# Optimization experiments

Measured on AMD Instinct MI355X. Metric: run time of the kernel, lower is better.

## Reference

```python
import jax, jax.numpy as jnp
import numpy as np

NUM_GRAPHS = 4096


def setup_inputs() -> dict:
    key = jax.random.key(0)
    k1, k2, k3, k4, k5 = jax.random.split(key, 5)
    N, H = 500000, 256
    x = jax.random.normal(k1, (N, H), dtype=jnp.float32)
    batch = jnp.sort(jax.random.randint(k2, (N,), 0, NUM_GRAPHS, dtype=jnp.int64))
    # gate MLP: Linear(H, H//2) -> tanh -> Linear(H//2, 1)
    W1 = jax.random.normal(k3, (H, H // 2), dtype=jnp.float32) / np.sqrt(H)
    b1 = jnp.zeros((H // 2,), dtype=jnp.float32)
    W2 = jax.random.normal(k4, (H // 2, 1), dtype=jnp.float32) / np.sqrt(H // 2)
    b2 = jnp.zeros((1,), dtype=jnp.float32)
    return {"x": x, "batch": batch, "W1": W1, "b1": b1, "W2": W2, "b2": b2}


def reference(x, batch, W1, b1, W2, b2):
    # gate scores per node: (N,)
    h = jnp.tanh(x @ W1 + b1)
    scores = (h @ W2 + b2).squeeze(-1)
    # segment (per-graph) softmax over nodes
    seg_max = jax.ops.segment_max(scores, batch, num_segments=NUM_GRAPHS)
    # empty segments give -inf max; guard so gather stays finite
    seg_max = jnp.where(jnp.isfinite(seg_max), seg_max, 0.0)
    ex = jnp.exp(scores - seg_max[batch])
    seg_sum = jax.ops.segment_sum(ex, batch, num_segments=NUM_GRAPHS)
    weights = ex / seg_sum[batch]  # (N,)
    # weighted scatter-add pooling -> (B, H)
    pooled = jax.ops.segment_sum(weights[:, None] * x, batch, num_segments=NUM_GRAPHS)
    return pooled, weights
```

## Files before the change

kernel.cpp:

```cpp
#include <hip/hip_runtime.h>
#include <hip/hip_bf16.h>

#define NGRAPH 4096

typedef __attribute__((ext_vector_type(8))) short s16x8;
typedef __attribute__((ext_vector_type(4))) float f32x4;
typedef unsigned int u32;

__device__ inline short f2bf(float f) {
  unsigned u = __float_as_uint(f);
  unsigned r = u + 0x7fffu + ((u >> 16) & 1u);
  return (short)(r >> 16);
}

__global__ void prepack_w1(const float* __restrict__ W1, s16x8* __restrict__ w1p) {
  int t = blockIdx.x * 256 + threadIdx.x;
  int f = t >> 6, l = t & 63;
  int kt = f >> 3, ct = f & 7;
  int k0 = kt * 32 + ((l >> 4) * 8);
  int c  = ct * 16 + (l & 15);
  s16x8 v;
  #pragma unroll
  for (int e = 0; e < 8; ++e) v[e] = f2bf(W1[(k0 + e) * 128 + c]);
  w1p[f * 64 + l] = v;
}

__device__ inline long long getb(const void* b, int i, int is64) {
  if (is64) return ((const long long*)b)[i];
  return (long long)((const int*)b)[i];
}

__device__ inline int lowb(const void* b, int n, long long v, int is64) {
  int lo = 0, hi = n;
  while (lo < hi) {
    int mid = (lo + hi) >> 1;
    if (getb(b, mid, is64) < v) lo = mid + 1; else hi = mid;
  }
  return lo;
}

__device__ inline int batch_is64(const void* batch, int N) {
  int probe = ((N & 1) == 0) ? (N - 1) : (N - 2);
  return (((const int*)batch)[probe] == 0) ? 1 : 0;
}

__global__ void seg_offsets(const void* __restrict__ batch, int* __restrict__ offs, int N) {
  int g = blockIdx.x * 256 + threadIdx.x;
  const int is64 = batch_is64(batch, N);
  if (g <= NGRAPH) offs[g] = lowb(batch, N, (long long)g, is64);
}

__device__ inline float fast_tanh(float v) {
  v = fminf(fmaxf(v, -15.f), 15.f);
  float e = __expf(2.f * v);
  return __fdividef(e - 1.f, e + 1.f);
}

__device__ inline void dma16(const float* src, char* ldsdst) {
  __builtin_amdgcn_global_load_lds(
      (const __attribute__((address_space(1))) u32*)src,
      (__attribute__((address_space(3))) u32*)ldsdst,
      16, 0, 0);
}

__global__ __launch_bounds__(256, 2)
void gate_pool(const float* __restrict__ x, const int* __restrict__ offs,
               const float* __restrict__ b1, const float* __restrict__ W2,
               const float* __restrict__ b2p, const s16x8* __restrict__ w1p,
               float* __restrict__ pooled, float* __restrict__ expout,
               float* __restrict__ segsum, int N)
{
  __shared__ __align__(16) char tile[64 * 1024];
  __shared__ float sp[2][64];
  __shared__ float sw[64];

  const int tid = threadIdx.x;
  const int w = tid >> 6, l = tid & 63;
  const int colhalf = w & 1, wp = w >> 1;
  const int l15 = l & 15, lg = l >> 4;
  const int node0 = blockIdx.x * 64;

  #pragma unroll
  for (int i = 0; i < 16; ++i) {
    const int r = i * 4 + w;
    int grow = node0 + r;
    if (grow >= N) grow = N - 1;
    const float* src = x + (size_t)grow * 256 + ((l ^ (r & 7)) << 2);
    dma16(src, tile + r * 1024);
  }

  float b1v[4], w2v[4];
  #pragma unroll
  for (int ct = 0; ct < 4; ++ct) {
    int c = colhalf * 64 + ct * 16 + l15;
    b1v[ct] = b1[c];
    w2v[ct] = W2[c];
  }
  const float b2s = b2p[0];

  __syncthreads();

  {
    const int r0 = wp * 32 + l15;
    const int r1 = r0 + 16;
    const char* p0 = tile + r0 * 1024;
    const char* p1 = tile + r1 * 1024;
    const int s0 = (r0 & 7), s1 = (r1 & 7);

    f32x4 accA0 = {0.f,0.f,0.f,0.f}, accA1 = {0.f,0.f,0.f,0.f};
    f32x4 accA2 = {0.f,0.f,0.f,0.f}, accA3 = {0.f,0.f,0.f,0.f};
    f32x4 accB0 = {0.f,0.f,0.f,0.f}, accB1 = {0.f,0.f,0.f,0.f};
    f32x4 accB2 = {0.f,0.f,0.f,0.f}, accB3 = {0.f,0.f,0.f,0.f};
    #pragma unroll
    for (int kt = 0; kt < 8; ++kt) {
      const int cc = kt * 8 + lg * 2;
      float4 xa0 = *(const float4*)(p0 + (((cc    ) ^ s0) << 4));
      float4 xb0 = *(const float4*)(p0 + (((cc + 1) ^ s0) << 4));
      float4 xa1 = *(const float4*)(p1 + (((cc    ) ^ s1) << 4));
      float4 xb1 = *(const float4*)(p1 + (((cc + 1) ^ s1) << 4));
      const s16x8* wb = w1p + (kt * 8 + colhalf * 4) * 64 + l;
      s16x8 bf0 = wb[0], bf1 = wb[64], bf2 = wb[128], bf3 = wb[192];
      s16x8 a0, a1;
      a0[0] = f2bf(xa0.x); a0[1] = f2bf(xa0.y); a0[2] = f2bf(xa0.z); a0[3] = f2bf(xa0.w);
      a0[4] = f2bf(xb0.x); a0[5] = f2bf(xb0.y); a0[6] = f2bf(xb0.z); a0[7] = f2bf(xb0.w);
      a1[0] = f2bf(xa1.x); a1[1] = f2bf(xa1.y); a1[2] = f2bf(xa1.z); a1[3] = f2bf(xa1.w);
      a1[4] = f2bf(xb1.x); a1[5] = f2bf(xb1.y); a1[6] = f2bf(xb1.z); a1[7] = f2bf(xb1.w);
      accA0 = __builtin_amdgcn_mfma_f32_16x16x32_bf16(a0, bf0, accA0, 0, 0, 0);
      accA1 = __builtin_amdgcn_mfma_f32_16x16x32_bf16(a0, bf1, accA1, 0, 0, 0);
      accA2 = __builtin_amdgcn_mfma_f32_16x16x32_bf16(a0, bf2, accA2, 0, 0, 0);
      accA3 = __builtin_amdgcn_mfma_f32_16x16x32_bf16(a0, bf3, accA3, 0, 0, 0);
      accB0 = __builtin_amdgcn_mfma_f32_16x16x32_bf16(a1, bf0, accB0, 0, 0, 0);
      accB1 = __builtin_amdgcn_mfma_f32_16x16x32_bf16(a1, bf1, accB1, 0, 0, 0);
      accB2 = __builtin_amdgcn_mfma_f32_16x16x32_bf16(a1, bf2, accB2, 0, 0, 0);
      accB3 = __builtin_amdgcn_mfma_f32_16x16x32_bf16(a1, bf3, accB3, 0, 0, 0);
    }
    float partA[4], partB[4];
    #pragma unroll
    for (int r = 0; r < 4; ++r) {
      float init = colhalf ? 0.f : b2s;
      partA[r] = init
        + fast_tanh(accA0[r] + b1v[0]) * w2v[0]
        + fast_tanh(accA1[r] + b1v[1]) * w2v[1]
        + fast_tanh(accA2[r] + b1v[2]) * w2v[2]
        + fast_tanh(accA3[r] + b1v[3]) * w2v[3];
      partB[r] = init
        + fast_tanh(accB0[r] + b1v[0]) * w2v[0]
        + fast_tanh(accB1[r] + b1v[1]) * w2v[1]
        + fast_tanh(accB2[r] + b1v[2]) * w2v[2]
        + fast_tanh(accB3[r] + b1v[3]) * w2v[3];
    }
    #pragma unroll
    for (int m = 1; m <= 8; m <<= 1) {
      #pragma unroll
      for (int r = 0; r < 4; ++r) {
        partA[r] += __shfl_xor(partA[r], m, 64);
        partB[r] += __shfl_xor(partB[r], m, 64);
      }
    }
    if (l15 == 0) {
      #pragma unroll
      for (int r = 0; r < 4; ++r) {
        sp[colhalf][wp * 32      + lg * 4 + r] = partA[r];
        sp[colhalf][wp * 32 + 16 + lg * 4 + r] = partB[r];
      }
    }
  }
  __syncthreads();

  if (tid < 64) {
    int node = node0 + tid;
    float e = 0.f;
    if (node < N) {
      e = __expf(sp[0][tid] + sp[1][tid]);
      expout[node] = e;
    }
    sw[tid] = e;
  }
  __syncthreads();

  const int nmax = min(64, N - node0);
  int g;
  {
    int lo = 0, hi = NGRAPH - 1;
    while (lo < hi) {
      int mid = (lo + hi) >> 1;
      if (offs[mid + 1] <= node0) lo = mid + 1; else hi = mid;
    }
    g = lo;
  }
  const int ccb = tid >> 2, cib = (tid & 3) << 2;
  int r = 0;
  int nb = offs[g + 1];
  while (r < nmax) {
    const int rend = min(nb - node0, nmax);
    float pacc = 0.f, wsum = 0.f;
    for (; r + 8 <= rend; r += 8) {
      float xv[8], wv[8];
      #pragma unroll
      for (int u = 0; u < 8; ++u) {
        const int rr = r + u;
        xv[u] = *(const float*)(tile + rr * 1024 + (((ccb ^ (rr & 7)) << 4) | cib));
        wv[u] = sw[rr];
      }
      #pragma unroll
      for (int u = 0; u < 8; ++u) {
        pacc += wv[u] * xv[u];
        wsum += wv[u];
      }
    }
    for (; r < rend; ++r) {
      float wv = sw[r];
      pacc += wv * *(const float*)(tile + r * 1024 + (((ccb ^ (r & 7)) << 4) | cib));
      wsum += wv;
    }
    if (wsum > 0.f) {
      atomicAdd(&pooled[(size_t)g * 256 + tid], pacc);
      if (tid == 0) atomicAdd(&segsum[g], wsum);
    }
    if (rend >= nmax) break;
    ++g;
    nb = offs[g + 1];
  }
}

__global__ void finalize(float* __restrict__ pooled, float* __restrict__ wts,
                         const float* __restrict__ segsum,
                         const void* __restrict__ batch, int N)
{
  int f = blockIdx.x * 256 + threadIdx.x;
  if (f < NGRAPH * 256) {
    int g = f >> 8;
    float s = segsum[g];
    pooled[f] = (s > 0.f) ? pooled[f] / s : 0.f;
  } else {
    int n = f - NGRAPH * 256;
    if (n < N) {
      const int is64 = batch_is64(batch, N);
      int g = (int)getb(batch, n, is64);
      wts[n] = wts[n] / segsum[g];
    }
  }
}

extern "C" void kernel_launch(void* const* d_in, const int* in_sizes, int n_in,
                              void* d_out, int out_size, void* d_ws, size_t ws_size,
                              hipStream_t stream) {
  const float* x     = (const float*)d_in[0];
  const void*  batch = d_in[1];
  const float* W1    = (const float*)d_in[2];
  const float* b1    = (const float*)d_in[3];
  const float* W2    = (const float*)d_in[4];
  const float* b2    = (const float*)d_in[5];
  const int N = in_sizes[0] / 256;

  float* pooled = (float*)d_out;
  float* wout   = (float*)d_out + (size_t)NGRAPH * 256;
  s16x8* w1p    = (s16x8*)d_ws;
  int*   offs   = (int*)((char*)d_ws + 64 * 1024);
  float* segsum = (float*)((char*)d_ws + 96 * 1024);

  hipMemsetAsync(pooled, 0, (size_t)NGRAPH * 256 * sizeof(float), stream);
  hipMemsetAsync(segsum, 0, (size_t)NGRAPH * sizeof(float), stream);

  prepack_w1<<<16, 256, 0, stream>>>(W1, w1p);
  seg_offsets<<<17, 256, 0, stream>>>(batch, offs, N);
  gate_pool<<<(N + 63) / 64, 256, 0, stream>>>(x, offs, b1, W2, b2, w1p,
                                               pooled, wout, segsum, N);
  const int tot = NGRAPH * 256 + N;
  finalize<<<(tot + 255) / 256, 256, 0, stream>>>(pooled, wout, segsum, batch, N);
}
```

Baseline: 193.5 us.

## Make gate_pool persistent with double-buffered LDS prefetch of node tiles

Replaces the one-block-per-64-node grid with 256 persistent blocks that loop over tiles, prefetching the next x tile into a second 64KB LDS buffer via direct global-to-LDS loads while computing the current one. W1 bf16 fragments are hoisted into registers once per block instead of being reloaded every k-step. The aim is to hide global load latency and cut per-block setup cost. The trade-off is 128KB of LDS for one block per CU, a large register footprint, and hand-placed waitcnt and barriers. With only 256 blocks, a device with more CUs than that would leave some idle.

```diff
diff --git a/kernel.cpp b/kernel.cpp
--- a/kernel.cpp
+++ b/kernel.cpp
@@ -2,6 +2,7 @@
 #include <hip/hip_bf16.h>
 
 #define NGRAPH 4096
+#define NPERS  256
 
 typedef __attribute__((ext_vector_type(8))) short s16x8;
 typedef __attribute__((ext_vector_type(4))) float f32x4;
@@ -63,14 +64,14 @@
       16, 0, 0);
 }
 
-__global__ __launch_bounds__(256, 2)
+__global__ __launch_bounds__(256, 1)
 void gate_pool(const float* __restrict__ x, const int* __restrict__ offs,
                const float* __restrict__ b1, const float* __restrict__ W2,
                const float* __restrict__ b2p, const s16x8* __restrict__ w1p,
                float* __restrict__ pooled, float* __restrict__ expout,
-               float* __restrict__ segsum, int N)
+               float* __restrict__ segsum, int N, int ntiles)
 {
-  __shared__ __align__(16) char tile[64 * 1024];
+  __shared__ __align__(16) char buf[2][64 * 1024];
   __shared__ float sp[2][64];
   __shared__ float sw[64];
 
@@ -78,16 +79,16 @@
   const int w = tid >> 6, l = tid & 63;
   const int colhalf = w & 1, wp = w >> 1;
   const int l15 = l & 15, lg = l >> 4;
-  const int node0 = blockIdx.x * 64;
-
+  const int bid = blockIdx.x;
+
+  if (bid >= ntiles) return;
+
+  s16x8 bf[4][8];
   #pragma unroll
-  for (int i = 0; i < 16; ++i) {
-    const int r = i * 4 + w;
-    int grow = node0 + r;
-    if (grow >= N) grow = N - 1;
-    const float* src = x + (size_t)grow * 256 + ((l ^ (r & 7)) << 2);
-    dma16(src, tile + r * 1024);
-  }
+  for (int ctl = 0; ctl < 4; ++ctl)
+    #pragma unroll
+    for (int kt = 0; kt < 8; ++kt)
+      bf[ctl][kt] = w1p[(kt * 8 + colhalf * 4 + ctl) * 64 + l];
 
   float b1v[4], w2v[4];
   #pragma unroll
@@ -98,128 +99,169 @@
   }
   const float b2s = b2p[0];
 
-  __syncthreads();
-
   {
-    const int r0 = wp * 32 + l15;
-    const int r1 = r0 + 16;
-    const char* p0 = tile + r0 * 1024;
-    const char* p1 = tile + r1 * 1024;
-    const int s0 = (r0 & 7), s1 = (r1 & 7);
-
-    f32x4 accA0 = {0.f,0.f,0.f,0.f}, accA1 = {0.f,0.f,0.f,0.f};
-    f32x4 accA2 = {0.f,0.f,0.f,0.f}, accA3 = {0.f,0.f,0.f,0.f};
-    f32x4 accB0 = {0.f,0.f,0.f,0.f}, accB1 = {0.f,0.f,0.f,0.f};
-    f32x4 accB2 = {0.f,0.f,0.f,0.f}, accB3 = {0.f,0.f,0.f,0.f};
+    const int node0 = bid * 64;
     #pragma unroll
-    for (int kt = 0; kt < 8; ++kt) {
-      const int cc = kt * 8 + lg * 2;
-      float4 xa0 = *(const float4*)(p0 + (((cc    ) ^ s0) << 4));
-      float4 xb0 = *(const float4*)(p0 + (((cc + 1) ^ s0) << 4));
-      float4 xa1 = *(const float4*)(p1 + (((cc    ) ^ s1) << 4));
-      float4 xb1 = *(const float4*)(p1 + (((cc + 1) ^ s1) << 4));
-      const s16x8* wb = w1p + (kt * 8 + colhalf * 4) * 64 + l;
-      s16x8 bf0 = wb[0], bf1 = wb[64], bf2 = wb[128], bf3 = wb[192];
-      s16x8 a0, a1;
-      a0[0] = f2bf(xa0.x); a0[1] = f2bf(xa0.y); a0[2] = f2bf(xa0.z); a0[3] = f2bf(xa0.w);
-      a0[4] = f2bf(xb0.x); a0[5] = f2bf(xb0.y); a0[6] = f2bf(xb0.z); a0[7] = f2bf(xb0.w);
-      a1[0] = f2bf(xa1.x); a1[1] = f2bf(xa1.y); a1[2] = f2bf(xa1.z); a1[3] = f2bf(xa1.w);
-      a1[4] = f2bf(xb1.x); a1[5] = f2bf(xb1.y); a1[6] = f2bf(xb1.z); a1[7] = f2bf(xb1.w);
-      accA0 = __builtin_amdgcn_mfma_f32_16x16x32_bf16(a0, bf0, accA0, 0, 0, 0);
-      accA1 = __builtin_amdgcn_mfma_f32_16x16x32_bf16(a0, bf1, accA1, 0, 0, 0);
-      accA2 = __builtin_amdgcn_mfma_f32_16x16x32_bf16(a0, bf2, accA2, 0, 0, 0);
-      accA3 = __builtin_amdgcn_mfma_f32_16x16x32_bf16(a0, bf3, accA3, 0, 0, 0);
-      accB0 = __builtin_amdgcn_mfma_f32_16x16x32_bf16(a1, bf0, accB0, 0, 0, 0);
-      accB1 = __builtin_amdgcn_mfma_f32_16x16x32_bf16(a1, bf1, accB1, 0, 0, 0);
-      accB2 = __builtin_amdgcn_mfma_f32_16x16x32_bf16(a1, bf2, accB2, 0, 0, 0);
-      accB3 = __builtin_amdgcn_mfma_f32_16x16x32_bf16(a1, bf3, accB3, 0, 0, 0);
-    }
-    float partA[4], partB[4];
-    #pragma unroll
-    for (int r = 0; r < 4; ++r) {
-      float init = colhalf ? 0.f : b2s;
-      partA[r] = init
-        + fast_tanh(accA0[r] + b1v[0]) * w2v[0]
-        + fast_tanh(accA1[r] + b1v[1]) * w2v[1]
-        + fast_tanh(accA2[r] + b1v[2]) * w2v[2]
-        + fast_tanh(accA3[r] + b1v[3]) * w2v[3];
-      partB[r] = init
-        + fast_tanh(accB0[r] + b1v[0]) * w2v[0]
-        + fast_tanh(accB1[r] + b1v[1]) * w2v[1]
-        + fast_tanh(accB2[r] + b1v[2]) * w2v[2]
-        + fast_tanh(accB3[r] + b1v[3]) * w2v[3];
-    }
-    #pragma unroll
-    for (int m = 1; m <= 8; m <<= 1) {
+    for (int i2 = 0; i2 < 16; ++i2) {
+      const int r = i2 * 4 + w;
+      int grow = node0 + r;
+      if (grow >= N) grow = N - 1;
+      dma16(x + (size_t)grow * 256 + ((l ^ (r & 7)) << 2), buf[0] + r * 1024);
+    }
+  }
+
+  int i = 0;
+  for (int ti = bid; ti < ntiles; ti += NPERS, ++i) {
+    const int cur = i & 1;
+    const int node0 = ti * 64;
+    const int tin = ti + NPERS;
+
+    if (tin < ntiles) {
+      const int nn0 = tin * 64;
+      char* dst = buf[cur ^ 1];
+      #pragma unroll
+      for (int i2 = 0; i2 < 16; ++i2) {
+        const int r = i2 * 4 + w;
+        int grow = nn0 + r;
+        if (grow >= N) grow = N - 1;
+        dma16(x + (size_t)grow * 256 + ((l ^ (r & 7)) << 2), dst + r * 1024);
+      }
+      asm volatile("s_waitcnt vmcnt(16)" ::: "memory");
+    } else {
+      asm volatile("s_waitcnt vmcnt(0)" ::: "memory");
+    }
+    __builtin_amdgcn_s_barrier();
+    __builtin_amdgcn_sched_barrier(0);
+
+    const char* tile = buf[cur];
+
+    {
+      const int r0 = wp * 32 + l15;
+      const int r1 = r0 + 16;
+      const char* p0 = tile + r0 * 1024;
+      const char* p1 = tile + r1 * 1024;
+      const int s0 = (r0 & 7), s1 = (r1 & 7);
+
+      f32x4 accA0 = {0.f,0.f,0.f,0.f}, accA1 = {0.f,0.f,0.f,0.f};
+      f32x4 accA2 = {0.f,0.f,0.f,0.f}, accA3 = {0.f,0.f,0.f,0.f};
+      f32x4 accB0 = {0.f,0.f,0.f,0.f}, accB1 = {0.f,0.f,0.f,0.f};
+      f32x4 accB2 = {0.f,0.f,0.f,0.f}, accB3 = {0.f,0.f,0.f,0.f};
+      #pragma unroll
+      for (int kt = 0; kt < 8; ++kt) {
+        const int cc = kt * 8 + lg * 2;
+        float4 xa0 = *(const float4*)(p0 + (((cc    ) ^ s0) << 4));
+        float4 xb0 = *(const float4*)(p0 + (((cc + 1) ^ s0) << 4));
+        float4 xa1 = *(const float4*)(p1 + (((cc    ) ^ s1) << 4));
+        float4 xb1 = *(const float4*)(p1 + (((cc + 1) ^ s1) << 4));
+        s16x8 a0, a1;
+        a0[0] = f2bf(xa0.x); a0[1] = f2bf(xa0.y); a0[2] = f2bf(xa0.z); a0[3] = f2bf(xa0.w);
+        a0[4] = f2bf(xb0.x); a0[5] = f2bf(xb0.y); a0[6] = f2bf(xb0.z); a0[7] = f2bf(xb0.w);
+        a1[0] = f2bf(xa1.x); a1[1] = f2bf(xa1.y); a1[2] = f2bf(xa1.z); a1[3] = f2bf(xa1.w);
+        a1[4] = f2bf(xb1.x); a1[5] = f2bf(xb1.y); a1[6] = f2bf(xb1.z); a1[7] = f2bf(xb1.w);
+        accA0 = __builtin_amdgcn_mfma_f32_16x16x32_bf16(a0, bf[0][kt], accA0, 0, 0, 0);
+        accA1 = __builtin_amdgcn_mfma_f32_16x16x32_bf16(a0, bf[1][kt], accA1, 0, 0, 0);
+        accA2 = __builtin_amdgcn_mfma_f32_16x16x32_bf16(a0, bf[2][kt], accA2, 0, 0, 0);
+        accA3 = __builtin_amdgcn_mfma_f32_16x16x32_bf16(a0, bf[3][kt], accA3, 0, 0, 0);
+        accB0 = __builtin_amdgcn_mfma_f32_16x16x32_bf16(a1, bf[0][kt], accB0, 0, 0, 0);
+        accB1 = __builtin_amdgcn_mfma_f32_16x16x32_bf16(a1, bf[1][kt], accB1, 0, 0, 0);
+        accB2 = __builtin_amdgcn_mfma_f32_16x16x32_bf16(a1, bf[2][kt], accB2, 0, 0, 0);
+        accB3 = __builtin_amdgcn_mfma_f32_16x16x32_bf16(a1, bf[3][kt], accB3, 0, 0, 0);
+      }
+      float partA[4], partB[4];
       #pragma unroll
       for (int r = 0; r < 4; ++r) {
-        partA[r] += __shfl_xor(partA[r], m, 64);
-        partB[r] += __shfl_xor(partB[r], m, 64);
-      }
-    }
-    if (l15 == 0) {
+        float init = colhalf ? 0.f : b2s;
+        partA[r] = init
+          + fast_tanh(accA0[r] + b1v[0]) * w2v[0]
+          + fast_tanh(accA1[r] + b1v[1]) * w2v[1]
+          + fast_tanh(accA2[r] + b1v[2]) * w2v[2]
+          + fast_tanh(accA3[r] + b1v[3]) * w2v[3];
+        partB[r] = init
+          + fast_tanh(accB0[r] + b1v[0]) * w2v[0]
+          + fast_tanh(accB1[r] + b1v[1]) * w2v[1]
+          + fast_tanh(accB2[r] + b1v[2]) * w2v[2]
+          + fast_tanh(accB3[r] + b1v[3]) * w2v[3];
+      }
       #pragma unroll
-      for (int r = 0; r < 4; ++r) {
-        sp[colhalf][wp * 32      + lg * 4 + r] = partA[r];
-        sp[colhalf][wp * 32 + 16 + lg * 4 + r] = partB[r];
-      }
-    }
-  }
-  __syncthreads();
-
-  if (tid < 64) {
-    int node = node0 + tid;
-    float e = 0.f;
-    if (node < N) {
-      e = __expf(sp[0][tid] + sp[1][tid]);
-      expout[node] = e;
-    }
-    sw[tid] = e;
-  }
-  __syncthreads();
-
-  const int nmax = min(64, N - node0);
-  int g;
-  {
-    int lo = 0, hi = NGRAPH - 1;
-    while (lo < hi) {
-      int mid = (lo + hi) >> 1;
-      if (offs[mid + 1] <= node0) lo = mid + 1; else hi = mid;
-    }
-    g = lo;
-  }
-  const int ccb = tid >> 2, cib = (tid & 3) << 2;
-  int r = 0;
-  int nb = offs[g + 1];
-  while (r < nmax) {
-    const int rend = min(nb - node0, nmax);
-    float pacc = 0.f, wsum = 0.f;
-    for (; r + 8 <= rend; r += 8) {
-      float xv[8], wv[8];
-      #pragma unroll
-      for (int u = 0; u < 8; ++u) {
-        const int rr = r + u;
-        xv[u] = *(const float*)(tile + rr * 1024 + (((ccb ^ (rr & 7)) << 4) | cib));
-        wv[u] = sw[rr];
-      }
-      #pragma unroll
-      for (int u = 0; u < 8; ++u) {
-        pacc += wv[u] * xv[u];
-        wsum += wv[u];
-      }
-    }
-    for (; r < rend; ++r) {
-      float wv = sw[r];
-      pacc += wv * *(const float*)(tile + r * 1024 + (((ccb ^ (r & 7)) << 4) | cib));
-      wsum += wv;
-    }
-    if (wsum > 0.f) {
-      atomicAdd(&pooled[(size_t)g * 256 + tid], pacc);
-      if (tid == 0) atomicAdd(&segsum[g], wsum);
-    }
-    if (rend >= nmax) break;
-    ++g;
-    nb = offs[g + 1];
+      for (int m = 1; m <= 8; m <<= 1) {
+        #pragma unroll
+        for (int r = 0; r < 4; ++r) {
+          partA[r] += __shfl_xor(partA[r], m, 64);
+          partB[r] += __shfl_xor(partB[r], m, 64);
+        }
+      }
+      if (l15 == 0) {
+        #pragma unroll
+        for (int r = 0; r < 4; ++r) {
+          sp[colhalf][wp * 32      + lg * 4 + r] = partA[r];
+          sp[colhalf][wp * 32 + 16 + lg * 4 + r] = partB[r];
+        }
+      }
+    }
+    asm volatile("s_waitcnt lgkmcnt(0)" ::: "memory");
+    __builtin_amdgcn_s_barrier();
+    __builtin_amdgcn_sched_barrier(0);
+
+    if (tid < 64) {
+      int node = node0 + tid;
+      float e = 0.f;
+      if (node < N) {
+        e = __expf(sp[0][tid] + sp[1][tid]);
+        expout[node] = e;
+      }
+      sw[tid] = e;
+    }
+    asm volatile("s_waitcnt lgkmcnt(0)" ::: "memory");
+    __builtin_amdgcn_s_barrier();
+    __builtin_amdgcn_sched_barrier(0);
+
+    {
+      const int nmax = min(64, N - node0);
+      int g;
+      {
+        int lo = 0, hi = NGRAPH - 1;
+        while (lo < hi) {
+          int mid = (lo + hi) >> 1;
+          if (offs[mid + 1] <= node0) lo = mid + 1; else hi = mid;
+        }
+        g = lo;
+      }
+      const int ccb = tid >> 2, cib = (tid & 3) << 2;
+      int r = 0;
+      int nb = offs[g + 1];
+      while (r < nmax) {
+        const int rend = min(nb - node0, nmax);
+        float pacc = 0.f, wsum = 0.f;
+        for (; r + 8 <= rend; r += 8) {
+          float xv[8], wv[8];
+          #pragma unroll
+          for (int u = 0; u < 8; ++u) {
+            const int rr = r + u;
+            xv[u] = *(const float*)(tile + rr * 1024 + (((ccb ^ (rr & 7)) << 4) | cib));
+            wv[u] = sw[rr];
+          }
+          #pragma unroll
+          for (int u = 0; u < 8; ++u) {
+            pacc += wv[u] * xv[u];
+            wsum += wv[u];
+          }
+        }
+        for (; r < rend; ++r) {
+          float wv = sw[r];
+          pacc += wv * *(const float*)(tile + r * 1024 + (((ccb ^ (r & 7)) << 4) | cib));
+          wsum += wv;
+        }
+        if (wsum > 0.f) {
+          atomicAdd(&pooled[(size_t)g * 256 + tid], pacc);
+          if (tid == 0) atomicAdd(&segsum[g], wsum);
+        }
+        if (rend >= nmax) break;
+        ++g;
+        nb = offs[g + 1];
+      }
+    }
+    __builtin_amdgcn_s_barrier();
+    __builtin_amdgcn_sched_barrier(0);
   }
 }
 
@@ -252,6 +294,7 @@
   const float* W2    = (const float*)d_in[4];
   const float* b2    = (const float*)d_in[5];
   const int N = in_sizes[0] / 256;
+  const int ntiles = (N + 63) / 64;
 
   float* pooled = (float*)d_out;
   float* wout   = (float*)d_out + (size_t)NGRAPH * 256;
@@ -264,8 +307,8 @@
 
   prepack_w1<<<16, 256, 0, stream>>>(W1, w1p);
   seg_offsets<<<17, 256, 0, stream>>>(batch, offs, N);
-  gate_pool<<<(N + 63) / 64, 256, 0, stream>>>(x, offs, b1, W2, b2, w1p,
-                                               pooled, wout, segsum, N);
+  gate_pool<<<NPERS, 256, 0, stream>>>(x, offs, b1, W2, b2, w1p,
+                                       pooled, wout, segsum, N, ntiles);
   const int tot = NGRAPH * 256 + N;
   finalize<<<(tot + 255) / 256, 256, 0, stream>>>(pooled, wout, segsum, batch, N);
 }
```

Result: slower. 268.9 us (+39.0%).
